# Kernel optimization log

Measured on AMD Instinct MI355X. Metric: run time of the kernel, lower is better.

The kernel has to match this reference:

```python
import jax, jax.numpy as jnp
import numpy as np

NUM_CAPS = 16; PLANES = 16; CAPS_SIZE = 16; NUM_CLASSES = 10
MAT = 4; ITERS = 3; FINAL_LAMBDA = 1e-2; EPS = 1e-8; BN_EPS = 1e-5
LN_2PI = float(np.log(2.0 * np.pi))


def _conv(x, w, pad):
    return jax.lax.conv_general_dilated(x, w, (1, 1), ((pad, pad), (pad, pad)),
                                        dimension_numbers=('NCHW', 'OIHW', 'NCHW'))


def _bn(x, g, b, m, v):
    # inference-mode BatchNorm2d
    scale = g / jnp.sqrt(v + BN_EPS)
    return (x - m[None, :, None, None]) * scale[None, :, None, None] + b[None, :, None, None]


def _unfold(x, k, stride, pad):
    # torch F.unfold ordering: [b, c, k*k, l]
    b, c, h, w = x.shape
    xp = jnp.pad(x, ((0, 0), (0, 0), (pad, pad), (pad, pad)))
    oh = (h + 2 * pad - k) // stride + 1
    ow = (w + 2 * pad - k) // stride + 1
    cols = jnp.stack([xp[:, :, i:i + stride * (oh - 1) + 1:stride, j:j + stride * (ow - 1) + 1:stride]
                      for i in range(k) for j in range(k)], axis=2)  # [b,c,kk,oh,ow]
    return cols.reshape(b, c, k * k, oh * ow), oh, ow


def em_routing(a, pose, W, beta_u, beta_a, k, stride, pad, A, B, P):
    mat = int(P ** 0.5); b = a.shape[0]; kk = k * k
    pc, oh, ow = _unfold(pose, k, stride, pad)          # [b, A*P, kk, l]
    l = oh * ow
    pc = pc.reshape(b, A, P, kk, l)
    pc = jnp.transpose(pc, (0, 4, 3, 1, 2)).reshape(b, l, kk * A, mat, mat)
    # votes: [b, l, kkA, B, P]
    v = jnp.einsum('blkih,kohj->blkoij', pc, W).reshape(b, l, kk * A, B, P)
    ac, _, _ = _unfold(a, k, stride, pad)               # [b, A, kk, l]
    a_in = jnp.transpose(ac.reshape(b, A, kk, l), (0, 3, 2, 1)).reshape(b, l, kk * A, 1)
    bu = beta_u.reshape(1, 1, 1, B, 1)
    ba = beta_a.reshape(1, 1, 1, B)
    r = jnp.full((b, l, kk * A, B), 1.0 / B, dtype=a.dtype)
    for it in range(ITERS):
        lam = FINAL_LAMBDA * (1.0 - 0.95 ** (it + 1))
        # ---- M step ----
        rw = r * a_in
        rw = rw / (jnp.sum(rw, axis=3, keepdims=True) + EPS)
        r_sum = jnp.sum(rw, axis=2, keepdims=True)            # [b,l,1,B]
        coeff = (rw / (r_sum + EPS))[..., None]
        mu = jnp.sum(coeff * v, axis=2, keepdims=True)        # [b,l,1,B,P]
        sig = jnp.sum(coeff * (v - mu) ** 2, axis=2, keepdims=True) + EPS
        cost = (bu + 0.5 * jnp.log(sig)) * r_sum[..., None]
        a_out = jax.nn.sigmoid(lam * (ba - jnp.sum(cost, axis=4)))  # [b,l,1,B]
        # ---- E step ----
        if it < ITERS - 1:
            ln_p = -0.5 * (v - mu) ** 2 / sig - 0.5 * jnp.log(sig) - 0.5 * LN_2PI
            r = jax.nn.softmax(jnp.sum(ln_p, axis=4) + jnp.log(a_out), axis=3)
    a_map = jnp.transpose(a_out.reshape(b, oh, ow, B), (0, 3, 1, 2))
    pose_map = jnp.transpose(mu.reshape(b, oh, ow, B * P), (0, 3, 1, 2))
    return a_map, pose_map


def setup_inputs() -> dict:
    key = jax.random.key(0)
    ks = jax.random.split(key, 24)
    Bt = 32; C_in = NUM_CAPS * PLANES  # 256
    d = {}
    d['x'] = jax.random.normal(ks[0], (Bt, C_in, 8, 8), jnp.float32)
    d['conv_a_w'] = jax.random.normal(ks[1], (NUM_CAPS, C_in, 3, 3), jnp.float32) * 0.03
    d['conv_pose_w'] = jax.random.normal(ks[2], (NUM_CAPS * CAPS_SIZE, C_in, 3, 3), jnp.float32) * 0.03

    def bn_params(k1, k2, c):
        return (jnp.ones((c,), jnp.float32), jnp.zeros((c,), jnp.float32),
                jax.random.normal(k1, (c,), jnp.float32) * 0.1,
                1.0 + 0.1 * jax.random.uniform(k2, (c,), jnp.float32))
    d['bn_a_g'], d['bn_a_b'], d['bn_a_m'], d['bn_a_v'] = bn_params(ks[3], ks[4], NUM_CAPS)
    d['bn_pose_g'], d['bn_pose_b'], d['bn_pose_m'], d['bn_pose_v'] = bn_params(ks[5], ks[6], NUM_CAPS * CAPS_SIZE)
    kkA = 9 * NUM_CAPS
    d['em0_W'] = jax.random.uniform(ks[7], (kkA, NUM_CAPS, MAT, MAT), jnp.float32, -0.5, 0.5)
    d['em0_bu'] = jax.random.normal(ks[8], (NUM_CAPS,), jnp.float32) * 0.01
    d['em0_ba'] = jax.random.normal(ks[9], (NUM_CAPS,), jnp.float32) * 0.01
    d['bn0_g'], d['bn0_b'], d['bn0_m'], d['bn0_v'] = bn_params(ks[10], ks[11], NUM_CAPS * CAPS_SIZE)
    d['em1_W'] = jax.random.uniform(ks[12], (kkA, NUM_CAPS, MAT, MAT), jnp.float32, -0.5, 0.5)
    d['em1_bu'] = jax.random.normal(ks[13], (NUM_CAPS,), jnp.float32) * 0.01
    d['em1_ba'] = jax.random.normal(ks[14], (NUM_CAPS,), jnp.float32) * 0.01
    d['bn1_g'], d['bn1_b'], d['bn1_m'], d['bn1_v'] = bn_params(ks[15], ks[16], NUM_CAPS * CAPS_SIZE)
    d['fc_W'] = jax.random.uniform(ks[17], (16 * NUM_CAPS, NUM_CLASSES, MAT, MAT), jnp.float32, -0.5, 0.5)
    d['fc_bu'] = jax.random.normal(ks[18], (NUM_CLASSES,), jnp.float32) * 0.01
    d['fc_ba'] = jax.random.normal(ks[19], (NUM_CLASSES,), jnp.float32) * 0.01
    return d


def reference(x, conv_a_w, conv_pose_w, bn_a_g, bn_a_b, bn_a_m, bn_a_v,
              bn_pose_g, bn_pose_b, bn_pose_m, bn_pose_v,
              em0_W, em0_bu, em0_ba, bn0_g, bn0_b, bn0_m, bn0_v,
              em1_W, em1_bu, em1_ba, bn1_g, bn1_b, bn1_m, bn1_v,
              fc_W, fc_bu, fc_ba):
    a = jax.nn.sigmoid(_bn(_conv(x, conv_a_w, 1), bn_a_g, bn_a_b, bn_a_m, bn_a_v))
    pose = _bn(_conv(x, conv_pose_w, 1), bn_pose_g, bn_pose_b, bn_pose_m, bn_pose_v)
    a, pose = em_routing(a, pose, em0_W, em0_bu, em0_ba, 3, 1, 1, NUM_CAPS, NUM_CAPS, CAPS_SIZE)
    pose = _bn(pose, bn0_g, bn0_b, bn0_m, bn0_v)
    a, pose = em_routing(a, pose, em1_W, em1_bu, em1_ba, 3, 1, 1, NUM_CAPS, NUM_CAPS, CAPS_SIZE)
    pose = _bn(pose, bn1_g, bn1_b, bn1_m, bn1_v)
    a, _ = em_routing(a, pose, fc_W, fc_bu, fc_ba, 4, 1, 0, NUM_CAPS, NUM_CLASSES, CAPS_SIZE)
    return jnp.mean(a, axis=(2, 3))  # [B, num_classes]
```

## Files before the change

kernel.cpp:

```cpp
#include <hip/hip_runtime.h>

#define EPSV 1e-8f
#define BN_EPS 1e-5f
#define LN_2PI 1.8378770664093453f

__device__ __forceinline__ float sigmoidf_(float x) { return 1.0f / (1.0f + expf(-x)); }

template<int C>
__device__ __forceinline__ float dppx(float x) {
    int i = __builtin_amdgcn_mov_dpp(__builtin_bit_cast(int, x), C, 0xF, 0xF, true);
    return __builtin_bit_cast(float, i);
}

template<int NACC>
__global__ __launch_bounds__(256, 4) void k_conv3(
    const float* __restrict__ x, const float* __restrict__ w,
    const float* __restrict__ g, const float* __restrict__ b_,
    const float* __restrict__ m, const float* __restrict__ v,
    float* __restrict__ out, int OC, int nOcg, int nIcq, int icChunk)
{
    __shared__ float xs[32 * 120];
    const int t = threadIdx.x;
    const int per_b = nOcg * nIcq;
    const int bidx = blockIdx.x / per_b;
    const int rem = blockIdx.x - bidx * per_b;
    const int ocg = rem / nIcq;
    const int icq = rem - ocg * nIcq;
    const int pix = t & 63, py = pix >> 3, px = pix & 7;
    const int ocb_u = __builtin_amdgcn_readfirstlane(t >> 6);
    const int ic0 = icq * icChunk;

    const int cells = icChunk * 120;
    for (int idx = t; idx < cells; idx += 256) {
        int icl = idx / 120;
        int c = idx - icl * 120;
        int iy = c / 12, ix = c - iy * 12;
        float val = 0.f;
        if (iy >= 1 && iy <= 8 && ix >= 1 && ix <= 8)
            val = x[(bidx * 256 + ic0 + icl) * 64 + (iy - 1) * 8 + (ix - 1)];
        xs[idx] = val;
    }
    __syncthreads();

    const int oc_base = ocg * 4 * NACC + ocb_u;
    const float* wb = w + ((size_t)(oc_base * 256 + ic0)) * 9;

    float acc[NACC];
    #pragma unroll
    for (int q = 0; q < NACC; ++q) acc[q] = 0.f;

    for (int icl = 0; icl < icChunk; ++icl) {
        const float* xr = &xs[icl * 120 + py * 12 + px];
        const float* wr = &wb[icl * 9];
        #pragma unroll
        for (int ky = 0; ky < 3; ++ky)
            #pragma unroll
            for (int kx = 0; kx < 3; ++kx) {
                float xv = xr[ky * 12 + kx];
                #pragma unroll
                for (int q = 0; q < NACC; ++q)
                    acc[q] = fmaf(wr[q * 9216 + ky * 3 + kx], xv, acc[q]);
            }
    }
    #pragma unroll
    for (int q = 0; q < NACC; ++q) {
        int oc = oc_base + 4 * q;
        float sc = g[oc] * rsqrtf(v[oc] + BN_EPS);
        float add = acc[q] * sc;
        if (icq == 0) add += b_[oc] - m[oc] * sc;
        atomicAdd(&out[(bidx * OC + oc) * 64 + pix], add);
    }
}

__global__ void k_sig(float* __restrict__ a, int n)
{
    int i = blockIdx.x * 256 + threadIdx.x;
    if (i < n) a[i] = 1.f / (1.f + expf(-a[i]));
}

__global__ __launch_bounds__(768) void k_em_conv(
    const float* __restrict__ a_in, const float* __restrict__ pose_in,
    const float* __restrict__ W, const float* __restrict__ bu, const float* __restrict__ ba,
    const float* __restrict__ bng, const float* __restrict__ bnb,
    const float* __restrict__ bnm, const float* __restrict__ bnv,
    float* __restrict__ a_out_g, float* __restrict__ pose_out)
{
    __shared__ float2 red2[3264] __attribute__((aligned(16)));
    __shared__ float prsum[192];
    __shared__ float a_s[160];
    __shared__ float2 mi_s[272];
    __shared__ float cst0_s[16], aout_s[16], laout_s[16];

    const int t = threadIdx.x;
    const int bidx = blockIdx.x >> 6;
    const int l = blockIdx.x & 63;
    const int y = l >> 3, xo = l & 7;
    const int kgl = t & 3;
    const int o = (t >> 2) & 15;
    const int w_id = t >> 6;
    const int kg = w_id * 4 + kgl;

    float* pc_s = reinterpret_cast<float*>(red2);

    for (int idx = t; idx < 2304; idx += 768) {
        int k = idx >> 4, p = idx & 15;
        int a = k & 15, kk = k >> 4;
        int iy = y + kk / 3 - 1, ix = xo + (kk % 3) - 1;
        float val = 0.f;
        if (iy >= 0 && iy < 8 && ix >= 0 && ix < 8)
            val = pose_in[(bidx * 256 + a * 16 + p) * 64 + iy * 8 + ix];
        pc_s[k * 20 + p] = val;
    }
    if (t < 144) {
        int a = t & 15, kk = t >> 4;
        int iy = y + kk / 3 - 1, ix = xo + (kk % 3) - 1;
        a_s[t] = (iy >= 0 && iy < 8 && ix >= 0 && ix < 8) ? a_in[(bidx * 16 + a) * 64 + iy * 8 + ix] : 0.f;
    }
    __syncthreads();

    float v[3][16];
    const float4* W4 = reinterpret_cast<const float4*>(W);
    #pragma unroll
    for (int s = 0; s < 3; ++s) {
        int k = kg + 48 * s;
        float pcl[16];
        #pragma unroll
        for (int c = 0; c < 4; ++c) {
            float4 p4 = *reinterpret_cast<const float4*>(&pc_s[k * 20 + c * 4]);
            pcl[c * 4 + 0] = p4.x; pcl[c * 4 + 1] = p4.y; pcl[c * 4 + 2] = p4.z; pcl[c * 4 + 3] = p4.w;
        }
        #pragma unroll
        for (int p = 0; p < 16; ++p) v[s][p] = 0.f;
        #pragma unroll
        for (int h = 0; h < 4; ++h) {
            float4 wr = W4[(k * 16 + o) * 4 + h];
            #pragma unroll
            for (int i = 0; i < 4; ++i) {
                float a = pcl[i * 4 + h];
                v[s][i * 4 + 0] = fmaf(a, wr.x, v[s][i * 4 + 0]);
                v[s][i * 4 + 1] = fmaf(a, wr.y, v[s][i * 4 + 1]);
                v[s][i * 4 + 2] = fmaf(a, wr.z, v[s][i * 4 + 2]);
                v[s][i * 4 + 3] = fmaf(a, wr.w, v[s][i * 4 + 3]);
            }
        }
    }
    float afac[3];
    #pragma unroll
    for (int s = 0; s < 3; ++s) { float av = a_s[kg + 48 * s]; afac[s] = av / (av + EPSV); }
    __syncthreads();

    float lg[3] = {0.f, 0.f, 0.f};
    for (int it = 0; it < 3; ++it) {
        float lam = (it == 0) ? 5.0e-4f : ((it == 1) ? 9.75e-4f : 1.42625e-3f);
        float rw[3];
        if (it == 0) {
            #pragma unroll
            for (int s = 0; s < 3; ++s) rw[s] = 0.0625f * afac[s];
        } else {
            #pragma unroll
            for (int s = 0; s < 3; ++s) {
                float mx = lg[s];
                #pragma unroll
                for (int mk = 4; mk <= 32; mk <<= 1) mx = fmaxf(mx, __shfl_xor(mx, mk, 64));
                float e = expf(lg[s] - mx);
                float den = e;
                #pragma unroll
                for (int mk = 4; mk <= 32; mk <<= 1) den += __shfl_xor(den, mk, 64);
                rw[s] = (e / den) * afac[s];
            }
        }
        float prw = rw[0] + rw[1] + rw[2];
        prw += dppx<0xB1>(prw); prw += dppx<0x4E>(prw);
        const int row = (w_id * 16 + o) * 17;
        if (kgl == 0) prsum[w_id * 16 + o] = prw;
        #pragma unroll
        for (int p = 0; p < 16; ++p) {
            float v0 = v[0][p], v1 = v[1][p], v2 = v[2][p];
            float pmp = rw[0] * v0; pmp = fmaf(rw[1], v1, pmp); pmp = fmaf(rw[2], v2, pmp);
            float pqp = rw[0] * v0 * v0; pqp = fmaf(rw[1] * v1, v1, pqp); pqp = fmaf(rw[2] * v2, v2, pqp);
            pmp += dppx<0xB1>(pmp); pmp += dppx<0x4E>(pmp);
            pqp += dppx<0xB1>(pqp); pqp += dppx<0x4E>(pqp);
            if (kgl == 0) red2[row + p] = make_float2(pmp, pqp);
        }
        __syncthreads();
        if (t < 256) {
            int oo = t >> 4, p = t & 15;
            float spm = 0.f, spq = 0.f, srs = 0.f;
            #pragma unroll
            for (int u = 0; u < 12; ++u) {
                float2 r2 = red2[(u * 16 + oo) * 17 + p];
                spm += r2.x; spq += r2.y;
                srs += prsum[u * 16 + oo];
            }
            float invr = 1.f / (srs + EPSV);
            float mu = spm * invr;
            float beta = srs * invr;
            float sig = fmaf(-(2.f - beta) * mu, mu, spq * invr) + EPSV;
            float ls = logf(sig);
            mi_s[oo * 17 + p] = make_float2(mu, 1.f / sig);
            float sumls = ls;
            #pragma unroll
            for (int mk = 1; mk <= 8; mk <<= 1) sumls += __shfl_xor(sumls, mk, 64);
            if (p == 0) {
                float cost = srs * fmaf(0.5f, sumls, 16.f * bu[oo]);
                float ao = sigmoidf_(lam * (ba[oo] - cost));
                aout_s[oo] = ao; laout_s[oo] = logf(ao);
                cst0_s[oo] = fmaf(-0.5f, sumls, -8.f * LN_2PI);
            }
        }
        __syncthreads();
        if (it < 2) {
            float s0 = 0.f, s1 = 0.f, s2 = 0.f;
            #pragma unroll
            for (int p = 0; p < 16; ++p) {
                float2 mi = mi_s[o * 17 + p];
                float d0 = v[0][p] - mi.x; s0 = fmaf(d0 * d0, mi.y, s0);
                float d1 = v[1][p] - mi.x; s1 = fmaf(d1 * d1, mi.y, s1);
                float d2 = v[2][p] - mi.x; s2 = fmaf(d2 * d2, mi.y, s2);
            }
            float cb = cst0_s[o] + laout_s[o];
            lg[0] = fmaf(-0.5f, s0, cb);
            lg[1] = fmaf(-0.5f, s1, cb);
            lg[2] = fmaf(-0.5f, s2, cb);
        }
    }
    if (t < 256) {
        float sc = bng[t] * rsqrtf(bnv[t] + BN_EPS);
        float mu = mi_s[(t >> 4) * 17 + (t & 15)].x;
        pose_out[(bidx * 256 + t) * 64 + l] = (mu - bnm[t]) * sc + bnb[t];
    }
    if (t < 16) a_out_g[(bidx * 16 + t) * 64 + l] = aout_s[t];
}

__global__ __launch_bounds__(640) void k_em_fc(
    const float* __restrict__ a_in, const float* __restrict__ pose_in,
    const float* __restrict__ W, const float* __restrict__ bu, const float* __restrict__ ba,
    float* __restrict__ out)
{
    __shared__ float red[10896] __attribute__((aligned(16)));
    __shared__ float rws[2816];
    __shared__ float ain_s[256];
    __shared__ float mu_s[176], lsig_s[176], isig_s[176];
    __shared__ float rs_s[16], aout_s[16], laout_s[16];

    const int t = threadIdx.x;
    const int bidx = blockIdx.x / 25;
    const int l = blockIdx.x % 25;
    const int y = l / 5, xo = l % 5;
    const int o = t >> 6;
    const int g = t & 63;

    float* pcs = red;
    for (int idx = t; idx < 4096; idx += 640) {
        int k = idx >> 4, p = idx & 15;
        int a = k & 15, kk = k >> 4;
        int iy = y + (kk >> 2), ix = xo + (kk & 3);
        pcs[k * 20 + p] = pose_in[((bidx * 256 + a * 16 + p) << 6) + iy * 8 + ix];
    }
    if (t < 256) {
        int a = t & 15, kk = t >> 4;
        int iy = y + (kk >> 2), ix = xo + (kk & 3);
        ain_s[t] = a_in[((bidx * 16 + a) << 6) + iy * 8 + ix];
    }
    __syncthreads();

    float v[4][16];
    const float4* W4 = reinterpret_cast<const float4*>(W);
    #pragma unroll
    for (int s = 0; s < 4; ++s) {
        int k = g + 64 * s;
        float pcl[16];
        #pragma unroll
        for (int c = 0; c < 4; ++c) {
            float4 p4 = *reinterpret_cast<const float4*>(&pcs[k * 20 + c * 4]);
            pcl[c * 4 + 0] = p4.x; pcl[c * 4 + 1] = p4.y; pcl[c * 4 + 2] = p4.z; pcl[c * 4 + 3] = p4.w;
        }
        #pragma unroll
        for (int p = 0; p < 16; ++p) v[s][p] = 0.f;
        #pragma unroll
        for (int h = 0; h < 4; ++h) {
            float4 wr = W4[(k * 10 + o) * 4 + h];
            #pragma unroll
            for (int i = 0; i < 4; ++i) {
                float a = pcl[i * 4 + h];
                v[s][i * 4 + 0] = fmaf(a, wr.x, v[s][i * 4 + 0]);
                v[s][i * 4 + 1] = fmaf(a, wr.y, v[s][i * 4 + 1]);
                v[s][i * 4 + 2] = fmaf(a, wr.z, v[s][i * 4 + 2]);
                v[s][i * 4 + 3] = fmaf(a, wr.w, v[s][i * 4 + 3]);
            }
        }
    }
    __syncthreads();

    const int rowb = t * 17 + o;
    for (int it = 0; it < 3; ++it) {
        float lam = (it == 0) ? 5.0e-4f : ((it == 1) ? 9.75e-4f : 1.42625e-3f);
        if (t < 256) {
            float av = ain_s[t];
            if (it == 0) {
                float val = 0.1f * av / (av + EPSV);
                #pragma unroll
                for (int oo = 0; oo < 10; ++oo) rws[t * 11 + oo] = val;
            } else {
                float mx = -1e30f;
                #pragma unroll
                for (int oo = 0; oo < 10; ++oo) mx = fmaxf(mx, rws[t * 11 + oo]);
                float den = 0.f;
                #pragma unroll
                for (int oo = 0; oo < 10; ++oo) den += expf(rws[t * 11 + oo] - mx);
                float sc = av / (den * (av + EPSV));
                #pragma unroll
                for (int oo = 0; oo < 10; ++oo) rws[t * 11 + oo] = expf(rws[t * 11 + oo] - mx) * sc;
            }
        }
        __syncthreads();
        float rwl[4]; float prs = 0.f;
        #pragma unroll
        for (int s = 0; s < 4; ++s) { rwl[s] = rws[(g + 64 * s) * 11 + o]; prs += rwl[s]; }
        #pragma unroll
        for (int off = 32; off > 0; off >>= 1) prs += __shfl_xor(prs, off, 64);
        if (g == 0) rs_s[o] = prs;
        #pragma unroll
        for (int p = 0; p < 16; ++p) {
            float pmp = rwl[0] * v[0][p];
            pmp = fmaf(rwl[1], v[1][p], pmp);
            pmp = fmaf(rwl[2], v[2][p], pmp);
            pmp = fmaf(rwl[3], v[3][p], pmp);
            red[rowb + p] = pmp;
        }
        __syncthreads();
        if (t < 160) {
            int oo = t >> 4, p = t & 15;
            float ssum = 0.f;
            #pragma unroll 8
            for (int gg = 0; gg < 64; ++gg) ssum += red[(oo * 64 + gg) * 17 + oo + p];
            mu_s[oo * 17 + p] = ssum / (rs_s[oo] + EPSV);
        }
        __syncthreads();
        #pragma unroll
        for (int p = 0; p < 16; ++p) {
            float ml = mu_s[o * 17 + p];
            float d0 = v[0][p] - ml; float pqp = rwl[0] * d0 * d0;
            float d1 = v[1][p] - ml; pqp = fmaf(rwl[1] * d1, d1, pqp);
            float d2 = v[2][p] - ml; pqp = fmaf(rwl[2] * d2, d2, pqp);
            float d3 = v[3][p] - ml; pqp = fmaf(rwl[3] * d3, d3, pqp);
            red[rowb + p] = pqp;
        }
        __syncthreads();
        if (t < 160) {
            int oo = t >> 4, p = t & 15;
            float ssum = 0.f;
            #pragma unroll 8
            for (int gg = 0; gg < 64; ++gg) ssum += red[(oo * 64 + gg) * 17 + oo + p];
            float sig = ssum / (rs_s[oo] + EPSV) + EPSV;
            float ls = logf(sig);
            lsig_s[oo * 17 + p] = ls;
            isig_s[oo * 17 + p] = 1.f / sig;
            float cost = (bu[oo] + 0.5f * ls) * rs_s[oo];
            #pragma unroll
            for (int mk = 1; mk <= 8; mk <<= 1) cost += __shfl_xor(cost, mk, 16);
            if (p == 0) {
                float ao = sigmoidf_(lam * (ba[oo] - cost));
                aout_s[oo] = ao; laout_s[oo] = logf(ao);
            }
        }
        __syncthreads();
        if (it < 2) {
            float s0 = 0.f, s1 = 0.f, s2 = 0.f, s3 = 0.f;
            float cst = -8.f * LN_2PI;
            #pragma unroll
            for (int p = 0; p < 16; ++p) {
                float ml = mu_s[o * 17 + p];
                float isg = isig_s[o * 17 + p];
                cst -= 0.5f * lsig_s[o * 17 + p];
                float d0 = v[0][p] - ml; s0 = fmaf(d0 * d0, isg, s0);
                float d1 = v[1][p] - ml; s1 = fmaf(d1 * d1, isg, s1);
                float d2 = v[2][p] - ml; s2 = fmaf(d2 * d2, isg, s2);
                float d3 = v[3][p] - ml; s3 = fmaf(d3 * d3, isg, s3);
            }
            const float la = laout_s[o];
            rws[(g      ) * 11 + o] = fmaf(-0.5f, s0, cst) + la;
            rws[(g +  64) * 11 + o] = fmaf(-0.5f, s1, cst) + la;
            rws[(g + 128) * 11 + o] = fmaf(-0.5f, s2, cst) + la;
            rws[(g + 192) * 11 + o] = fmaf(-0.5f, s3, cst) + la;
        }
        __syncthreads();
    }
    if (t < 10) atomicAdd(&out[bidx * 10 + t], aout_s[t] * 0.04f);
}

extern "C" void kernel_launch(void* const* d_in, const int* in_sizes, int n_in,
                              void* d_out, int out_size, void* d_ws, size_t ws_size,
                              hipStream_t stream)
{
    const float* x           = (const float*)d_in[0];
    const float* conv_a_w    = (const float*)d_in[1];
    const float* conv_pose_w = (const float*)d_in[2];
    const float* bn_a_g = (const float*)d_in[3];
    const float* bn_a_b = (const float*)d_in[4];
    const float* bn_a_m = (const float*)d_in[5];
    const float* bn_a_v = (const float*)d_in[6];
    const float* bn_p_g = (const float*)d_in[7];
    const float* bn_p_b = (const float*)d_in[8];
    const float* bn_p_m = (const float*)d_in[9];
    const float* bn_p_v = (const float*)d_in[10];
    const float* em0_W  = (const float*)d_in[11];
    const float* em0_bu = (const float*)d_in[12];
    const float* em0_ba = (const float*)d_in[13];
    const float* bn0_g  = (const float*)d_in[14];
    const float* bn0_b  = (const float*)d_in[15];
    const float* bn0_m  = (const float*)d_in[16];
    const float* bn0_v  = (const float*)d_in[17];
    const float* em1_W  = (const float*)d_in[18];
    const float* em1_bu = (const float*)d_in[19];
    const float* em1_ba = (const float*)d_in[20];
    const float* bn1_g  = (const float*)d_in[21];
    const float* bn1_b  = (const float*)d_in[22];
    const float* bn1_m  = (const float*)d_in[23];
    const float* bn1_v  = (const float*)d_in[24];
    const float* fc_W   = (const float*)d_in[25];
    const float* fc_bu  = (const float*)d_in[26];
    const float* fc_ba  = (const float*)d_in[27];

    float* ws    = (float*)d_ws;
    float* a0    = ws;
    float* pose0 = a0 + 32768;
    float* a1    = pose0 + 524288;
    float* pose1 = a1 + 32768;
    float* a2    = pose1 + 524288;
    float* pose2 = a2 + 32768;
    float* out   = (float*)d_out;

    hipMemsetAsync(d_out, 0, (size_t)out_size * sizeof(float), stream);
    hipMemsetAsync(a0, 0, (size_t)(32768 + 524288) * sizeof(float), stream);
    k_conv3<4><<<256, 256, 0, stream>>>(x, conv_a_w, bn_a_g, bn_a_b, bn_a_m, bn_a_v,
                                        a0, 16, 1, 8, 32);
    k_conv3<8><<<2048, 256, 0, stream>>>(x, conv_pose_w, bn_p_g, bn_p_b, bn_p_m, bn_p_v,
                                         pose0, 256, 8, 8, 32);
    k_sig<<<128, 256, 0, stream>>>(a0, 32768);
    k_em_conv<<<2048, 768, 0, stream>>>(a0, pose0, em0_W, em0_bu, em0_ba,
                                        bn0_g, bn0_b, bn0_m, bn0_v, a1, pose1);
    k_em_conv<<<2048, 768, 0, stream>>>(a1, pose1, em1_W, em1_bu, em1_ba,
                                        bn1_g, bn1_b, bn1_m, bn1_v, a2, pose2);
    k_em_fc<<<800, 640, 0, stream>>>(a2, pose2, fc_W, fc_bu, fc_ba, out);
}
```

Baseline: 513.8 us.

## Use packed float2 math in EM kernels and wave-level reduce-scatter in FC routing

Vote computation and the M/E-step arithmetic in both EM kernels are rewritten with 2-wide float vectors so the compiler can emit packed FP32 instructions. The FC routing kernel replaces its shared-memory two-pass reduction with a register reduce-scatter across lanes within each wave. It computes mean and second moment in a single pass and evaluates the activation per wave, which removes several block-wide barriers and the large reduction buffer. Occupancy hints are also added to the launch bounds. The single-pass variance trades some numerical robustness for fewer syncs, and the new occupancy hints may force register spills.

Measured after the change: 684.8 us. 33.3% more time.

```diff
diff --git a/kernel.cpp b/kernel.cpp
--- a/kernel.cpp
+++ b/kernel.cpp
@@ -3,6 +3,9 @@
 #define EPSV 1e-8f
 #define BN_EPS 1e-5f
 #define LN_2PI 1.8378770664093453f
+
+typedef float v2f __attribute__((ext_vector_type(2)));
+__device__ __forceinline__ v2f splat2(float x) { v2f r; r.x = x; r.y = x; return r; }
 
 __device__ __forceinline__ float sigmoidf_(float x) { return 1.0f / (1.0f + expf(-x)); }
 
@@ -10,6 +13,46 @@
 __device__ __forceinline__ float dppx(float x) {
     int i = __builtin_amdgcn_mov_dpp(__builtin_bit_cast(int, x), C, 0xF, 0xF, true);
     return __builtin_bit_cast(float, i);
+}
+
+__device__ __forceinline__ float rscat16(float cur[16], int g) {
+    {
+        const bool hi = (g & 32) != 0;
+        #pragma unroll
+        for (int i = 0; i < 8; ++i) {
+            float send = hi ? cur[i] : cur[i + 8];
+            float keep = hi ? cur[i + 8] : cur[i];
+            cur[i] = keep + __shfl_xor(send, 32, 64);
+        }
+    }
+    {
+        const bool hi = (g & 16) != 0;
+        #pragma unroll
+        for (int i = 0; i < 4; ++i) {
+            float send = hi ? cur[i] : cur[i + 4];
+            float keep = hi ? cur[i + 4] : cur[i];
+            cur[i] = keep + __shfl_xor(send, 16, 64);
+        }
+    }
+    {
+        const bool hi = (g & 8) != 0;
+        #pragma unroll
+        for (int i = 0; i < 2; ++i) {
+            float send = hi ? cur[i] : cur[i + 2];
+            float keep = hi ? cur[i + 2] : cur[i];
+            cur[i] = keep + __shfl_xor(send, 8, 64);
+        }
+    }
+    {
+        const bool hi = (g & 4) != 0;
+        float send = hi ? cur[0] : cur[1];
+        float keep = hi ? cur[1] : cur[0];
+        cur[0] = keep + __shfl_xor(send, 4, 64);
+    }
+    float r = cur[0];
+    r += __shfl_xor(r, 1, 64);
+    r += __shfl_xor(r, 2, 64);
+    return r;
 }
 
 template<int NACC>
@@ -78,17 +121,17 @@
     if (i < n) a[i] = 1.f / (1.f + expf(-a[i]));
 }
 
-__global__ __launch_bounds__(768) void k_em_conv(
+__global__ __launch_bounds__(768, 6) void k_em_conv(
     const float* __restrict__ a_in, const float* __restrict__ pose_in,
     const float* __restrict__ W, const float* __restrict__ bu, const float* __restrict__ ba,
     const float* __restrict__ bng, const float* __restrict__ bnb,
     const float* __restrict__ bnm, const float* __restrict__ bnv,
     float* __restrict__ a_out_g, float* __restrict__ pose_out)
 {
-    __shared__ float2 red2[3264] __attribute__((aligned(16)));
+    __shared__ float4 red4[192 * 9] __attribute__((aligned(16)));
     __shared__ float prsum[192];
     __shared__ float a_s[160];
-    __shared__ float2 mi_s[272];
+    __shared__ float mu_s[16 * 18], is_s[16 * 18];
     __shared__ float cst0_s[16], aout_s[16], laout_s[16];
 
     const int t = threadIdx.x;
@@ -100,7 +143,7 @@
     const int w_id = t >> 6;
     const int kg = w_id * 4 + kgl;
 
-    float* pc_s = reinterpret_cast<float*>(red2);
+    float* pc_s = reinterpret_cast<float*>(red4);
 
     for (int idx = t; idx < 2304; idx += 768) {
         int k = idx >> 4, p = idx & 15;
@@ -118,7 +161,7 @@
     }
     __syncthreads();
 
-    float v[3][16];
+    v2f v2[3][8];
     const float4* W4 = reinterpret_cast<const float4*>(W);
     #pragma unroll
     for (int s = 0; s < 3; ++s) {
@@ -130,17 +173,17 @@
             pcl[c * 4 + 0] = p4.x; pcl[c * 4 + 1] = p4.y; pcl[c * 4 + 2] = p4.z; pcl[c * 4 + 3] = p4.w;
         }
         #pragma unroll
-        for (int p = 0; p < 16; ++p) v[s][p] = 0.f;
+        for (int j = 0; j < 8; ++j) v2[s][j] = splat2(0.f);
         #pragma unroll
         for (int h = 0; h < 4; ++h) {
             float4 wr = W4[(k * 16 + o) * 4 + h];
+            v2f wa; wa.x = wr.x; wa.y = wr.y;
+            v2f wb; wb.x = wr.z; wb.y = wr.w;
             #pragma unroll
             for (int i = 0; i < 4; ++i) {
-                float a = pcl[i * 4 + h];
-                v[s][i * 4 + 0] = fmaf(a, wr.x, v[s][i * 4 + 0]);
-                v[s][i * 4 + 1] = fmaf(a, wr.y, v[s][i * 4 + 1]);
-                v[s][i * 4 + 2] = fmaf(a, wr.z, v[s][i * 4 + 2]);
-                v[s][i * 4 + 3] = fmaf(a, wr.w, v[s][i * 4 + 3]);
+                v2f a2 = splat2(pcl[i * 4 + h]);
+                v2[s][i * 2]     += a2 * wa;
+                v2[s][i * 2 + 1] += a2 * wb;
             }
         }
     }
@@ -171,25 +214,32 @@
         }
         float prw = rw[0] + rw[1] + rw[2];
         prw += dppx<0xB1>(prw); prw += dppx<0x4E>(prw);
-        const int row = (w_id * 16 + o) * 17;
         if (kgl == 0) prsum[w_id * 16 + o] = prw;
-        #pragma unroll
-        for (int p = 0; p < 16; ++p) {
-            float v0 = v[0][p], v1 = v[1][p], v2 = v[2][p];
-            float pmp = rw[0] * v0; pmp = fmaf(rw[1], v1, pmp); pmp = fmaf(rw[2], v2, pmp);
-            float pqp = rw[0] * v0 * v0; pqp = fmaf(rw[1] * v1, v1, pqp); pqp = fmaf(rw[2] * v2, v2, pqp);
-            pmp += dppx<0xB1>(pmp); pmp += dppx<0x4E>(pmp);
-            pqp += dppx<0xB1>(pqp); pqp += dppx<0x4E>(pqp);
-            if (kgl == 0) red2[row + p] = make_float2(pmp, pqp);
+        const int row4 = (w_id * 16 + o) * 9;
+        const v2f r0 = splat2(rw[0]), r1 = splat2(rw[1]), r2 = splat2(rw[2]);
+        #pragma unroll
+        for (int j = 0; j < 8; ++j) {
+            v2f a0 = v2[0][j], a1 = v2[1][j], a2 = v2[2][j];
+            v2f pm = r0 * a0 + r1 * a1 + r2 * a2;
+            v2f pq = r0 * (a0 * a0) + r1 * (a1 * a1) + r2 * (a2 * a2);
+            float pmx = pm.x, pmy = pm.y, pqx = pq.x, pqy = pq.y;
+            pmx += dppx<0xB1>(pmx); pmx += dppx<0x4E>(pmx);
+            pmy += dppx<0xB1>(pmy); pmy += dppx<0x4E>(pmy);
+            pqx += dppx<0xB1>(pqx); pqx += dppx<0x4E>(pqx);
+            pqy += dppx<0xB1>(pqy); pqy += dppx<0x4E>(pqy);
+            if (kgl == 0) red4[row4 + j] = make_float4(pmx, pmy, pqx, pqy);
         }
         __syncthreads();
         if (t < 256) {
             int oo = t >> 4, p = t & 15;
+            int jj = p >> 1, sel = p & 1;
+            const float* rf = reinterpret_cast<const float*>(red4);
             float spm = 0.f, spq = 0.f, srs = 0.f;
             #pragma unroll
             for (int u = 0; u < 12; ++u) {
-                float2 r2 = red2[(u * 16 + oo) * 17 + p];
-                spm += r2.x; spq += r2.y;
+                int base = ((u * 16 + oo) * 9 + jj) * 4;
+                spm += rf[base + sel];
+                spq += rf[base + 2 + sel];
                 srs += prsum[u * 16 + oo];
             }
             float invr = 1.f / (srs + EPSV);
@@ -197,7 +247,8 @@
             float beta = srs * invr;
             float sig = fmaf(-(2.f - beta) * mu, mu, spq * invr) + EPSV;
             float ls = logf(sig);
-            mi_s[oo * 17 + p] = make_float2(mu, 1.f / sig);
+            mu_s[oo * 18 + p] = mu;
+            is_s[oo * 18 + p] = 1.f / sig;
             float sumls = ls;
             #pragma unroll
             for (int mk = 1; mk <= 8; mk <<= 1) sumls += __shfl_xor(sumls, mk, 64);
@@ -210,38 +261,39 @@
         }
         __syncthreads();
         if (it < 2) {
-            float s0 = 0.f, s1 = 0.f, s2 = 0.f;
-            #pragma unroll
-            for (int p = 0; p < 16; ++p) {
-                float2 mi = mi_s[o * 17 + p];
-                float d0 = v[0][p] - mi.x; s0 = fmaf(d0 * d0, mi.y, s0);
-                float d1 = v[1][p] - mi.x; s1 = fmaf(d1 * d1, mi.y, s1);
-                float d2 = v[2][p] - mi.x; s2 = fmaf(d2 * d2, mi.y, s2);
+            const v2f* mu2 = reinterpret_cast<const v2f*>(&mu_s[o * 18]);
+            const v2f* is2 = reinterpret_cast<const v2f*>(&is_s[o * 18]);
+            v2f s0 = splat2(0.f), s1 = splat2(0.f), s2 = splat2(0.f);
+            #pragma unroll
+            for (int j = 0; j < 8; ++j) {
+                v2f m2 = mu2[j], iv = is2[j];
+                v2f d0 = v2[0][j] - m2; s0 += (d0 * d0) * iv;
+                v2f d1 = v2[1][j] - m2; s1 += (d1 * d1) * iv;
+                v2f d2 = v2[2][j] - m2; s2 += (d2 * d2) * iv;
             }
             float cb = cst0_s[o] + laout_s[o];
-            lg[0] = fmaf(-0.5f, s0, cb);
-            lg[1] = fmaf(-0.5f, s1, cb);
-            lg[2] = fmaf(-0.5f, s2, cb);
+            lg[0] = fmaf(-0.5f, s0.x + s0.y, cb);
+            lg[1] = fmaf(-0.5f, s1.x + s1.y, cb);
+            lg[2] = fmaf(-0.5f, s2.x + s2.y, cb);
         }
     }
     if (t < 256) {
         float sc = bng[t] * rsqrtf(bnv[t] + BN_EPS);
-        float mu = mi_s[(t >> 4) * 17 + (t & 15)].x;
+        float mu = mu_s[(t >> 4) * 18 + (t & 15)];
         pose_out[(bidx * 256 + t) * 64 + l] = (mu - bnm[t]) * sc + bnb[t];
     }
     if (t < 16) a_out_g[(bidx * 16 + t) * 64 + l] = aout_s[t];
 }
 
-__global__ __launch_bounds__(640) void k_em_fc(
+__global__ __launch_bounds__(640, 5) void k_em_fc(
     const float* __restrict__ a_in, const float* __restrict__ pose_in,
     const float* __restrict__ W, const float* __restrict__ bu, const float* __restrict__ ba,
     float* __restrict__ out)
 {
-    __shared__ float red[10896] __attribute__((aligned(16)));
+    __shared__ float pcs[5120];
     __shared__ float rws[2816];
     __shared__ float ain_s[256];
-    __shared__ float mu_s[176], lsig_s[176], isig_s[176];
-    __shared__ float rs_s[16], aout_s[16], laout_s[16];
+    __shared__ float mu_s[10 * 18], is_s[10 * 18];
 
     const int t = threadIdx.x;
     const int bidx = blockIdx.x / 25;
@@ -250,7 +302,6 @@
     const int o = t >> 6;
     const int g = t & 63;
 
-    float* pcs = red;
     for (int idx = t; idx < 4096; idx += 640) {
         int k = idx >> 4, p = idx & 15;
         int a = k & 15, kk = k >> 4;
@@ -264,7 +315,7 @@
     }
     __syncthreads();
 
-    float v[4][16];
+    v2f v2[4][8];
     const float4* W4 = reinterpret_cast<const float4*>(W);
     #pragma unroll
     for (int s = 0; s < 4; ++s) {
@@ -276,23 +327,25 @@
             pcl[c * 4 + 0] = p4.x; pcl[c * 4 + 1] = p4.y; pcl[c * 4 + 2] = p4.z; pcl[c * 4 + 3] = p4.w;
         }
         #pragma unroll
-        for (int p = 0; p < 16; ++p) v[s][p] = 0.f;
+        for (int j = 0; j < 8; ++j) v2[s][j] = splat2(0.f);
         #pragma unroll
         for (int h = 0; h < 4; ++h) {
             float4 wr = W4[(k * 10 + o) * 4 + h];
+            v2f wa; wa.x = wr.x; wa.y = wr.y;
+            v2f wb; wb.x = wr.z; wb.y = wr.w;
             #pragma unroll
             for (int i = 0; i < 4; ++i) {
-                float a = pcl[i * 4 + h];
-                v[s][i * 4 + 0] = fmaf(a, wr.x, v[s][i * 4 + 0]);
-                v[s][i * 4 + 1] = fmaf(a, wr.y, v[s][i * 4 + 1]);
-                v[s][i * 4 + 2] = fmaf(a, wr.z, v[s][i * 4 + 2]);
-                v[s][i * 4 + 3] = fmaf(a, wr.w, v[s][i * 4 + 3]);
-            }
-        }
-    }
-    __syncthreads();
-
-    const int rowb = t * 17 + o;
+                v2f a2 = splat2(pcl[i * 4 + h]);
+                v2[s][i * 2]     += a2 * wa;
+                v2[s][i * 2 + 1] += a2 * wb;
+            }
+        }
+    }
+
+    const float bu_o = bu[o], ba_o = ba[o];
+    const int myp = (g >> 2) & 15;
+    float aout_f = 0.f;
+
     for (int it = 0; it < 3; ++it) {
         float lam = (it == 0) ? 5.0e-4f : ((it == 1) ? 9.75e-4f : 1.42625e-3f);
         if (t < 256) {
@@ -314,79 +367,66 @@
             }
         }
         __syncthreads();
-        float rwl[4]; float prs = 0.f;
-        #pragma unroll
-        for (int s = 0; s < 4; ++s) { rwl[s] = rws[(g + 64 * s) * 11 + o]; prs += rwl[s]; }
-        #pragma unroll
-        for (int off = 32; off > 0; off >>= 1) prs += __shfl_xor(prs, off, 64);
-        if (g == 0) rs_s[o] = prs;
-        #pragma unroll
-        for (int p = 0; p < 16; ++p) {
-            float pmp = rwl[0] * v[0][p];
-            pmp = fmaf(rwl[1], v[1][p], pmp);
-            pmp = fmaf(rwl[2], v[2][p], pmp);
-            pmp = fmaf(rwl[3], v[3][p], pmp);
-            red[rowb + p] = pmp;
-        }
-        __syncthreads();
-        if (t < 160) {
-            int oo = t >> 4, p = t & 15;
-            float ssum = 0.f;
-            #pragma unroll 8
-            for (int gg = 0; gg < 64; ++gg) ssum += red[(oo * 64 + gg) * 17 + oo + p];
-            mu_s[oo * 17 + p] = ssum / (rs_s[oo] + EPSV);
-        }
-        __syncthreads();
-        #pragma unroll
-        for (int p = 0; p < 16; ++p) {
-            float ml = mu_s[o * 17 + p];
-            float d0 = v[0][p] - ml; float pqp = rwl[0] * d0 * d0;
-            float d1 = v[1][p] - ml; pqp = fmaf(rwl[1] * d1, d1, pqp);
-            float d2 = v[2][p] - ml; pqp = fmaf(rwl[2] * d2, d2, pqp);
-            float d3 = v[3][p] - ml; pqp = fmaf(rwl[3] * d3, d3, pqp);
-            red[rowb + p] = pqp;
-        }
-        __syncthreads();
-        if (t < 160) {
-            int oo = t >> 4, p = t & 15;
-            float ssum = 0.f;
-            #pragma unroll 8
-            for (int gg = 0; gg < 64; ++gg) ssum += red[(oo * 64 + gg) * 17 + oo + p];
-            float sig = ssum / (rs_s[oo] + EPSV) + EPSV;
-            float ls = logf(sig);
-            lsig_s[oo * 17 + p] = ls;
-            isig_s[oo * 17 + p] = 1.f / sig;
-            float cost = (bu[oo] + 0.5f * ls) * rs_s[oo];
-            #pragma unroll
-            for (int mk = 1; mk <= 8; mk <<= 1) cost += __shfl_xor(cost, mk, 16);
-            if (p == 0) {
-                float ao = sigmoidf_(lam * (ba[oo] - cost));
-                aout_s[oo] = ao; laout_s[oo] = logf(ao);
-            }
-        }
-        __syncthreads();
+        float rwl[4]; float rs = 0.f;
+        #pragma unroll
+        for (int s = 0; s < 4; ++s) { rwl[s] = rws[(g + 64 * s) * 11 + o]; rs += rwl[s]; }
+        #pragma unroll
+        for (int mk = 1; mk <= 32; mk <<= 1) rs += __shfl_xor(rs, mk, 64);
+        const float invr = 1.f / (rs + EPSV);
+        const float beta = rs * invr;
+        const v2f q0 = splat2(rwl[0]), q1 = splat2(rwl[1]), q2 = splat2(rwl[2]), q3 = splat2(rwl[3]);
+        float mu_p;
+        {
+            float cur[16];
+            #pragma unroll
+            for (int j = 0; j < 8; ++j) {
+                v2f pm = q0 * v2[0][j] + q1 * v2[1][j] + q2 * v2[2][j] + q3 * v2[3][j];
+                cur[2 * j] = pm.x; cur[2 * j + 1] = pm.y;
+            }
+            mu_p = rscat16(cur, g) * invr;
+        }
+        if ((g & 3) == 0) mu_s[o * 18 + myp] = mu_p;
+        float ls;
+        {
+            float cur[16];
+            #pragma unroll
+            for (int j = 0; j < 8; ++j) {
+                v2f a0 = v2[0][j], a1 = v2[1][j], a2 = v2[2][j], a3 = v2[3][j];
+                v2f pq = q0 * (a0 * a0) + q1 * (a1 * a1) + q2 * (a2 * a2) + q3 * (a3 * a3);
+                cur[2 * j] = pq.x; cur[2 * j + 1] = pq.y;
+            }
+            float E2 = rscat16(cur, g) * invr;
+            float sig = fmaf(-(2.f - beta) * mu_p, mu_p, E2) + EPSV;
+            ls = logf(sig);
+            if ((g & 3) == 0) is_s[o * 18 + myp] = 1.f / sig;
+        }
+        float sumls = ls;
+        #pragma unroll
+        for (int mk = 4; mk <= 32; mk <<= 1) sumls += __shfl_xor(sumls, mk, 64);
+        float cost = rs * fmaf(0.5f, sumls, 16.f * bu_o);
+        float ao = sigmoidf_(lam * (ba_o - cost));
+        if (it == 2) { aout_f = ao; }
         if (it < 2) {
-            float s0 = 0.f, s1 = 0.f, s2 = 0.f, s3 = 0.f;
-            float cst = -8.f * LN_2PI;
-            #pragma unroll
-            for (int p = 0; p < 16; ++p) {
-                float ml = mu_s[o * 17 + p];
-                float isg = isig_s[o * 17 + p];
-                cst -= 0.5f * lsig_s[o * 17 + p];
-                float d0 = v[0][p] - ml; s0 = fmaf(d0 * d0, isg, s0);
-                float d1 = v[1][p] - ml; s1 = fmaf(d1 * d1, isg, s1);
-                float d2 = v[2][p] - ml; s2 = fmaf(d2 * d2, isg, s2);
-                float d3 = v[3][p] - ml; s3 = fmaf(d3 * d3, isg, s3);
-            }
-            const float la = laout_s[o];
-            rws[(g      ) * 11 + o] = fmaf(-0.5f, s0, cst) + la;
-            rws[(g +  64) * 11 + o] = fmaf(-0.5f, s1, cst) + la;
-            rws[(g + 128) * 11 + o] = fmaf(-0.5f, s2, cst) + la;
-            rws[(g + 192) * 11 + o] = fmaf(-0.5f, s3, cst) + la;
-        }
-        __syncthreads();
-    }
-    if (t < 10) atomicAdd(&out[bidx * 10 + t], aout_s[t] * 0.04f);
+            float cst = fmaf(-0.5f, sumls, -8.f * LN_2PI) + logf(ao);
+            const v2f* mu2 = reinterpret_cast<const v2f*>(&mu_s[o * 18]);
+            const v2f* is2 = reinterpret_cast<const v2f*>(&is_s[o * 18]);
+            v2f s0 = splat2(0.f), s1 = splat2(0.f), s2 = splat2(0.f), s3 = splat2(0.f);
+            #pragma unroll
+            for (int j = 0; j < 8; ++j) {
+                v2f m2 = mu2[j], iv = is2[j];
+                v2f d0 = v2[0][j] - m2; s0 += (d0 * d0) * iv;
+                v2f d1 = v2[1][j] - m2; s1 += (d1 * d1) * iv;
+                v2f d2 = v2[2][j] - m2; s2 += (d2 * d2) * iv;
+                v2f d3 = v2[3][j] - m2; s3 += (d3 * d3) * iv;
+            }
+            rws[(g      ) * 11 + o] = fmaf(-0.5f, s0.x + s0.y, cst);
+            rws[(g +  64) * 11 + o] = fmaf(-0.5f, s1.x + s1.y, cst);
+            rws[(g + 128) * 11 + o] = fmaf(-0.5f, s2.x + s2.y, cst);
+            rws[(g + 192) * 11 + o] = fmaf(-0.5f, s3.x + s3.y, cst);
+            __syncthreads();
+        }
+    }
+    if (g == 0) atomicAdd(&out[bidx * 10 + o], aout_f * 0.04f);
 }
 
 extern "C" void kernel_launch(void* const* d_in, const int* in_sizes, int n_in,
```
